# Kernel tuning notes

Measured on AMD Instinct MI355X. Metric: run time of the kernel, lower is better.

Reference implementation:

```python
import jax, jax.numpy as jnp
import numpy as np

OUT, IN, BLK = 11008, 4096, 128

def setup_inputs() -> dict:
    key = jax.random.key(0)
    k1, k2, k3, k4, k5 = jax.random.split(key, 5)
    x = jax.random.normal(k1, (64, IN), dtype=jnp.float32)
    weight = jax.random.randint(k2, (OUT, IN // 2), 0, 256, dtype=jnp.int32)  # packed uint4 pairs
    scale = jax.random.uniform(k3, (OUT, 1, BLK), dtype=jnp.float32) * 0.01 + 1e-4
    zp = jax.random.randint(k4, (OUT, 1, BLK), 0, 16).astype(jnp.float32)
    bias = jax.random.normal(k5, (OUT,), dtype=jnp.float32)
    return {"x": x, "weight": weight, "scale": scale, "zp": zp, "bias": bias}

def reference(x, weight, scale, zp, bias):
    dtype = x.dtype
    # unpack: high nibble first, then low nibble (interleaved along in_features)
    w_h = (weight >> 4) & 15
    w_l = weight & 15
    w_unpacked = jnp.stack((w_h, w_l), axis=-1).reshape(OUT, IN)
    # block-wise dequant: scale/zp shaped [OUT, 1, BLK], broadcast over block index dim
    w_blocked = w_unpacked.reshape(OUT, IN // BLK, BLK).astype(dtype)
    w_rec = ((w_blocked - zp.astype(dtype)) * scale.astype(dtype)).reshape(OUT, IN)
    return x @ w_rec.T + bias
```

## Files before the change

### kernel.cpp

```cpp
#include <hip/hip_runtime.h>

#define OUT_F 11008
#define IN_F  4096
#define PKW   2048
#define BLKQ  128

typedef __attribute__((ext_vector_type(8))) short          s16x8;
typedef __attribute__((ext_vector_type(8))) unsigned short u16x8;
typedef __attribute__((ext_vector_type(4))) float          f32x4;
typedef __attribute__((ext_vector_type(4))) int            i32x4;

__device__ __forceinline__ unsigned short f2bf(float f) {
    union { float f; unsigned u; } v; v.f = f;
    unsigned r = v.u + 0x8000u + ((v.u >> 16) & 1u);
    return (unsigned short)(r >> 16);
}

__global__ void prep_xfrag(const float* __restrict__ x, unsigned short* __restrict__ xf) {
    int kb   = blockIdx.x;
    int t    = threadIdx.x;
    int mt   = t >> 6;
    int lane = t & 63;
    int m  = mt * 16 + (lane & 15);
    int k0 = kb * 32 + (lane >> 4) * 8;
    const float* xp = x + m * IN_F + k0;
    f32x4 a = *(const f32x4*)(xp);
    f32x4 b = *(const f32x4*)(xp + 4);
    u16x8 v;
    v[0] = f2bf(a[0]); v[1] = f2bf(a[1]); v[2] = f2bf(a[2]); v[3] = f2bf(a[3]);
    v[4] = f2bf(b[0]); v[5] = f2bf(b[1]); v[6] = f2bf(b[2]); v[7] = f2bf(b[3]);
    *(u16x8*)(xf + (size_t)((kb * 4 + mt) * 64 + lane) * 8) = v;
}

__global__ __launch_bounds__(256, 3) void qlin_main(
    const int*   __restrict__ wq,
    const float* __restrict__ scale,
    const float* __restrict__ zp,
    const float* __restrict__ bias,
    const unsigned short* __restrict__ xf,
    float* __restrict__ out)
{
    __shared__ float lsum[4 * 1024];

    const int t      = threadIdx.x;
    const int o_base = blockIdx.x * 16;
    const int wave   = t >> 6;
    const int lane   = t & 63;
    const int o_r    = lane & 15;
    const int quad   = lane >> 4;
    const int o      = o_base + o_r;

    float s[4][8], zs[4][8];
    {
        const float* sp  = scale + (size_t)o * BLKQ + quad * 8;
        const float* zpp = zp    + (size_t)o * BLKQ + quad * 8;
        #pragma unroll
        for (int c4 = 0; c4 < 4; ++c4) {
            f32x4 s0 = *(const f32x4*)(sp  + c4 * 32);
            f32x4 s1 = *(const f32x4*)(sp  + c4 * 32 + 4);
            f32x4 z0 = *(const f32x4*)(zpp + c4 * 32);
            f32x4 z1 = *(const f32x4*)(zpp + c4 * 32 + 4);
            #pragma unroll
            for (int i = 0; i < 4; ++i) {
                s [c4][i]     = s0[i];  zs[c4][i]     = z0[i] * s0[i];
                s [c4][i + 4] = s1[i];  zs[c4][i + 4] = z1[i] * s1[i];
            }
        }
    }

    const int* wb = wq + (size_t)o * PKW + wave * 512 + quad * 4;
    const s16x8* xfv = (const s16x8*)xf;
    const int kb0 = wave * 32;

    f32x4 acc[4];
    #pragma unroll
    for (int mt = 0; mt < 4; ++mt) acc[mt] = (f32x4){0.f, 0.f, 0.f, 0.f};

    i32x4 wgA[4], wgB[4];
    s16x8 afA[4], afB[4];

#define LOAD_WGRP(DST, GIDX) do {                                   \
        const int* nb_ = wb + (GIDX) * 64;                          \
        DST[0] = *(const i32x4*)(nb_);                              \
        DST[1] = *(const i32x4*)(nb_ + 16);                         \
        DST[2] = *(const i32x4*)(nb_ + 32);                         \
        DST[3] = *(const i32x4*)(nb_ + 48);                         \
    } while (0)

#define LOAD_AF(DST, KB) do {                                       \
        size_t b_ = (size_t)((KB) * 4) * 64 + lane;                 \
        DST[0] = xfv[b_];                                           \
        DST[1] = xfv[b_ + 64];                                      \
        DST[2] = xfv[b_ + 128];                                     \
        DST[3] = xfv[b_ + 192];                                     \
    } while (0)

#define DEQ_MFMA(W, CC, AFC, AFN, KBN, DOPREF) do {                              \
        if (DOPREF) LOAD_AF(AFN, (KBN));                                         \
        s16x8 bfr;                                                               \
        _Pragma("unroll")                                                        \
        for (int d = 0; d < 4; ++d) {                                            \
            unsigned dw = (unsigned)W[CC][d];                                    \
            float fh = (float)((dw >> 4) & 15u);       \
            float fl = (float)(dw & 15u);                             \
            bfr[2 * d]     = (short)f2bf(fmaf(fh, s[CC][2 * d],     -zs[CC][2 * d]));     \
            bfr[2 * d + 1] = (short)f2bf(fmaf(fl, s[CC][2 * d + 1], -zs[CC][2 * d + 1])); \
        }                                                                        \
        acc[0] = __builtin_amdgcn_mfma_f32_16x16x32_bf16(AFC[0], bfr, acc[0], 0, 0, 0); \
        acc[1] = __builtin_amdgcn_mfma_f32_16x16x32_bf16(AFC[1], bfr, acc[1], 0, 0, 0); \
        acc[2] = __builtin_amdgcn_mfma_f32_16x16x32_bf16(AFC[2], bfr, acc[2], 0, 0, 0); \
        acc[3] = __builtin_amdgcn_mfma_f32_16x16x32_bf16(AFC[3], bfr, acc[3], 0, 0, 0); \
    } while (0)

    LOAD_WGRP(wgA, 0);
    LOAD_AF(afA, kb0);

    for (int g = 0; g < 8; g += 2) {
        const int kw = kb0 + g * 4;
        LOAD_WGRP(wgB, g + 1);
        DEQ_MFMA(wgA, 0, afA, afB, kw + 1, 1);
        DEQ_MFMA(wgA, 1, afB, afA, kw + 2, 1);
        DEQ_MFMA(wgA, 2, afA, afB, kw + 3, 1);
        DEQ_MFMA(wgA, 3, afB, afA, kw + 4, 1);
        if (g + 2 < 8) LOAD_WGRP(wgA, g + 2);
        DEQ_MFMA(wgB, 0, afA, afB, kw + 5, 1);
        DEQ_MFMA(wgB, 1, afB, afA, kw + 6, 1);
        DEQ_MFMA(wgB, 2, afA, afB, kw + 7, 1);
        DEQ_MFMA(wgB, 3, afB, afA, kw + 8, (g + 2 < 8));
    }
#undef LOAD_WGRP
#undef LOAD_AF
#undef DEQ_MFMA

    #pragma unroll
    for (int mt = 0; mt < 4; ++mt) {
        #pragma unroll
        for (int r = 0; r < 4; ++r) {
            int m = mt * 16 + quad * 4 + r;
            lsum[wave * 1024 + m * 16 + o_r] = acc[mt][r];
        }
    }
    __syncthreads();
    #pragma unroll
    for (int p = 0; p < 4; ++p) {
        int e = p * 256 + t;
        int m = e >> 4, col = e & 15;
        float v = lsum[e] + lsum[1024 + e] + lsum[2048 + e] + lsum[3072 + e] + bias[o_base + col];
        out[(size_t)m * OUT_F + o_base + col] = v;
    }
}

extern "C" void kernel_launch(void* const* d_in, const int* in_sizes, int n_in,
                              void* d_out, int out_size, void* d_ws, size_t ws_size,
                              hipStream_t stream) {
    const float* x     = (const float*)d_in[0];
    const int*   wq    = (const int*)d_in[1];
    const float* scale = (const float*)d_in[2];
    const float* zpv   = (const float*)d_in[3];
    const float* bias  = (const float*)d_in[4];
    float* out = (float*)d_out;
    unsigned short* xf = (unsigned short*)d_ws;

    prep_xfrag<<<128, 256, 0, stream>>>(x, xf);
    qlin_main<<<OUT_F / 16, 256, 0, stream>>>(wq, scale, zpv, bias, xf, out);
}
```

Measured before the change: 162.0 us.

## Split K across eight waves with per-wave scale phase and deeper prefetch

```diff
diff --git a/kernel.cpp b/kernel.cpp
--- a/kernel.cpp
+++ b/kernel.cpp
@@ -32,7 +32,7 @@
     *(u16x8*)(xf + (size_t)((kb * 4 + mt) * 64 + lane) * 8) = v;
 }
 
-__global__ __launch_bounds__(256, 3) void qlin_main(
+__global__ __launch_bounds__(512, 4) void qlin_main(
     const int*   __restrict__ wq,
     const float* __restrict__ scale,
     const float* __restrict__ zp,
@@ -40,7 +40,7 @@
     const unsigned short* __restrict__ xf,
     float* __restrict__ out)
 {
-    __shared__ float lsum[4 * 1024];
+    __shared__ float lsum[8 * 1024];
 
     const int t      = threadIdx.x;
     const int o_base = blockIdx.x * 16;
@@ -49,103 +49,87 @@
     const int o_r    = lane & 15;
     const int quad   = lane >> 4;
     const int o      = o_base + o_r;
+    const int kh     = wave >> 2;
+    const int ph     = wave & 3;
 
-    float s[4][8], zs[4][8];
+    float s[8], zs[8];
     {
-        const float* sp  = scale + (size_t)o * BLKQ + quad * 8;
-        const float* zpp = zp    + (size_t)o * BLKQ + quad * 8;
+        const float* sp  = scale + (size_t)o * BLKQ + ph * 32 + quad * 8;
+        const float* zpp = zp    + (size_t)o * BLKQ + ph * 32 + quad * 8;
+        f32x4 s0 = *(const f32x4*)(sp);
+        f32x4 s1 = *(const f32x4*)(sp + 4);
+        f32x4 z0 = *(const f32x4*)(zpp);
+        f32x4 z1 = *(const f32x4*)(zpp + 4);
         #pragma unroll
-        for (int c4 = 0; c4 < 4; ++c4) {
-            f32x4 s0 = *(const f32x4*)(sp  + c4 * 32);
-            f32x4 s1 = *(const f32x4*)(sp  + c4 * 32 + 4);
-            f32x4 z0 = *(const f32x4*)(zpp + c4 * 32);
-            f32x4 z1 = *(const f32x4*)(zpp + c4 * 32 + 4);
-            #pragma unroll
-            for (int i = 0; i < 4; ++i) {
-                s [c4][i]     = s0[i];  zs[c4][i]     = z0[i] * s0[i];
-                s [c4][i + 4] = s1[i];  zs[c4][i + 4] = z1[i] * s1[i];
-            }
+        for (int i = 0; i < 4; ++i) {
+            s [i]     = s0[i];  zs[i]     = z0[i] * s0[i];
+            s [i + 4] = s1[i];  zs[i + 4] = z1[i] * s1[i];
         }
     }
 
-    const int* wb = wq + (size_t)o * PKW + wave * 512 + quad * 4;
-    const s16x8* xfv = (const s16x8*)xf;
-    const int kb0 = wave * 32;
+    const int* wqp = wq + (size_t)o * PKW + (kh * 64 + ph) * 16 + quad * 4;
+    const s16x8* xfp = (const s16x8*)xf + (size_t)(kh * 64 + ph) * 256 + lane;
 
-    f32x4 acc[4];
-    #pragma unroll
-    for (int mt = 0; mt < 4; ++mt) acc[mt] = (f32x4){0.f, 0.f, 0.f, 0.f};
+    f32x4 acc0 = {0.f,0.f,0.f,0.f}, acc1 = acc0, acc2 = acc0, acc3 = acc0;
+    s16x8 afA0, afA1, afA2, afA3, afB0, afB1, afB2, afB3;
+    i32x4 wg0, wg1, wg2, wg3;
 
-    i32x4 wgA[4], wgB[4];
-    s16x8 afA[4], afB[4];
+    afA0 = xfp[0];    afA1 = xfp[64];        afA2 = xfp[128];        afA3 = xfp[192];
+    afB0 = xfp[1024]; afB1 = xfp[1024 + 64]; afB2 = xfp[1024 + 128]; afB3 = xfp[1024 + 192];
+    wg0 = *(const i32x4*)(wqp);
+    wg1 = *(const i32x4*)(wqp + 64);
+    wg2 = *(const i32x4*)(wqp + 128);
+    wg3 = *(const i32x4*)(wqp + 192);
 
-#define LOAD_WGRP(DST, GIDX) do {                                   \
-        const int* nb_ = wb + (GIDX) * 64;                          \
-        DST[0] = *(const i32x4*)(nb_);                              \
-        DST[1] = *(const i32x4*)(nb_ + 16);                         \
-        DST[2] = *(const i32x4*)(nb_ + 32);                         \
-        DST[3] = *(const i32x4*)(nb_ + 48);                         \
-    } while (0)
-
-#define LOAD_AF(DST, KB) do {                                       \
-        size_t b_ = (size_t)((KB) * 4) * 64 + lane;                 \
-        DST[0] = xfv[b_];                                           \
-        DST[1] = xfv[b_ + 64];                                      \
-        DST[2] = xfv[b_ + 128];                                     \
-        DST[3] = xfv[b_ + 192];                                     \
-    } while (0)
-
-#define DEQ_MFMA(W, CC, AFC, AFN, KBN, DOPREF) do {                              \
-        if (DOPREF) LOAD_AF(AFN, (KBN));                                         \
+#define SUB(J, A0, A1, A2, A3) do {                                              \
         s16x8 bfr;                                                               \
         _Pragma("unroll")                                                        \
         for (int d = 0; d < 4; ++d) {                                            \
-            unsigned dw = (unsigned)W[CC][d];                                    \
+            unsigned dw = (unsigned)wg##J[d];                                    \
             float fh = (float)((dw >> 4) & 15u);       \
             float fl = (float)(dw & 15u);                             \
-            bfr[2 * d]     = (short)f2bf(fmaf(fh, s[CC][2 * d],     -zs[CC][2 * d]));     \
-            bfr[2 * d + 1] = (short)f2bf(fmaf(fl, s[CC][2 * d + 1], -zs[CC][2 * d + 1])); \
+            bfr[2 * d]     = (short)f2bf(fmaf(fh, s[2 * d],     -zs[2 * d]));    \
+            bfr[2 * d + 1] = (short)f2bf(fmaf(fl, s[2 * d + 1], -zs[2 * d + 1]));\
         }                                                                        \
-        acc[0] = __builtin_amdgcn_mfma_f32_16x16x32_bf16(AFC[0], bfr, acc[0], 0, 0, 0); \
-        acc[1] = __builtin_amdgcn_mfma_f32_16x16x32_bf16(AFC[1], bfr, acc[1], 0, 0, 0); \
-        acc[2] = __builtin_amdgcn_mfma_f32_16x16x32_bf16(AFC[2], bfr, acc[2], 0, 0, 0); \
-        acc[3] = __builtin_amdgcn_mfma_f32_16x16x32_bf16(AFC[3], bfr, acc[3], 0, 0, 0); \
+        acc0 = __builtin_amdgcn_mfma_f32_16x16x32_bf16(A0, bfr, acc0, 0, 0, 0);  \
+        acc1 = __builtin_amdgcn_mfma_f32_16x16x32_bf16(A1, bfr, acc1, 0, 0, 0);  \
+        acc2 = __builtin_amdgcn_mfma_f32_16x16x32_bf16(A2, bfr, acc2, 0, 0, 0);  \
+        acc3 = __builtin_amdgcn_mfma_f32_16x16x32_bf16(A3, bfr, acc3, 0, 0, 0);  \
+        if (tp + (J) + 2 < 16) {                                                 \
+            const s16x8* ap_ = xfp + (size_t)(tp + (J) + 2) * 1024;              \
+            A0 = ap_[0]; A1 = ap_[64]; A2 = ap_[128]; A3 = ap_[192];             \
+        }                                                                        \
+        if (tp + (J) + 4 < 16) {                                                 \
+            wg##J = *(const i32x4*)(wqp + (tp + (J) + 4) * 64);                  \
+        }                                                                        \
     } while (0)
 
-    LOAD_WGRP(wgA, 0);
-    LOAD_AF(afA, kb0);
+    for (int tp = 0; tp < 16; tp += 4) {
+        SUB(0, afA0, afA1, afA2, afA3);
+        SUB(1, afB0, afB1, afB2, afB3);
+        SUB(2, afA0, afA1, afA2, afA3);
+        SUB(3, afB0, afB1, afB2, afB3);
+    }
+#undef SUB
 
-    for (int g = 0; g < 8; g += 2) {
-        const int kw = kb0 + g * 4;
-        LOAD_WGRP(wgB, g + 1);
-        DEQ_MFMA(wgA, 0, afA, afB, kw + 1, 1);
-        DEQ_MFMA(wgA, 1, afB, afA, kw + 2, 1);
-        DEQ_MFMA(wgA, 2, afA, afB, kw + 3, 1);
-        DEQ_MFMA(wgA, 3, afB, afA, kw + 4, 1);
-        if (g + 2 < 8) LOAD_WGRP(wgA, g + 2);
-        DEQ_MFMA(wgB, 0, afA, afB, kw + 5, 1);
-        DEQ_MFMA(wgB, 1, afB, afA, kw + 6, 1);
-        DEQ_MFMA(wgB, 2, afA, afB, kw + 7, 1);
-        DEQ_MFMA(wgB, 3, afB, afA, kw + 8, (g + 2 < 8));
-    }
-#undef LOAD_WGRP
-#undef LOAD_AF
-#undef DEQ_MFMA
-
-    #pragma unroll
-    for (int mt = 0; mt < 4; ++mt) {
-        #pragma unroll
-        for (int r = 0; r < 4; ++r) {
-            int m = mt * 16 + quad * 4 + r;
-            lsum[wave * 1024 + m * 16 + o_r] = acc[mt][r];
-        }
+    {
+        const int mb = quad * 4;
+#define STACC(MT, A)                                                  \
+        lsum[wave * 1024 + ((MT) * 16 + mb + 0) * 16 + o_r] = A[0];   \
+        lsum[wave * 1024 + ((MT) * 16 + mb + 1) * 16 + o_r] = A[1];   \
+        lsum[wave * 1024 + ((MT) * 16 + mb + 2) * 16 + o_r] = A[2];   \
+        lsum[wave * 1024 + ((MT) * 16 + mb + 3) * 16 + o_r] = A[3];
+        STACC(0, acc0) STACC(1, acc1) STACC(2, acc2) STACC(3, acc3)
+#undef STACC
     }
     __syncthreads();
     #pragma unroll
-    for (int p = 0; p < 4; ++p) {
-        int e = p * 256 + t;
+    for (int p = 0; p < 2; ++p) {
+        int e = p * 512 + t;
         int m = e >> 4, col = e & 15;
-        float v = lsum[e] + lsum[1024 + e] + lsum[2048 + e] + lsum[3072 + e] + bias[o_base + col];
+        float v = lsum[e]        + lsum[1024 + e] + lsum[2048 + e] + lsum[3072 + e]
+                + lsum[4096 + e] + lsum[5120 + e] + lsum[6144 + e] + lsum[7168 + e]
+                + bias[o_base + col];
         out[(size_t)m * OUT_F + o_base + col] = v;
     }
 }
@@ -162,5 +146,5 @@
     unsigned short* xf = (unsigned short*)d_ws;
 
     prep_xfrag<<<128, 256, 0, stream>>>(x, xf);
-    qlin_main<<<OUT_F / 16, 256, 0, stream>>>(wq, scale, zpv, bias, xf, out);
+    qlin_main<<<OUT_F / 16, 512, 0, stream>>>(wq, scale, zpv, bias, xf, out);
 }
```

Result: slower. 169.1 us (+4.4%).
